# Kernel optimization log

Measured on AMD Instinct MI355X. Metric: run time of the kernel, lower is better.

## Reference

```python
import jax, jax.numpy as jnp
import numpy as np

B, N, P, K = 128, 256, 256, 4  # batches, obs points, pred points, nfunc


def setup_inputs() -> dict:
    key = jax.random.key(0)
    k1, k2, k3, k4, k5 = jax.random.split(key, 5)
    # squared distances: symmetric obs-obs block with zero diagonal + obs-pred block
    d_oo = jax.random.uniform(k1, (B, N, N), dtype=jnp.float32) * 25.0
    d_oo = 0.5 * (d_oo + jnp.swapaxes(d_oo, -1, -2))
    d_oo = d_oo * (1.0 - jnp.eye(N, dtype=jnp.float32))
    d_op = jax.random.uniform(k2, (B, N, P), dtype=jnp.float32) * 25.0
    C = jnp.concatenate([d_oo, d_op], axis=-1)  # (B, N, N+P)
    val = jax.random.normal(k3, (B, N, K), dtype=jnp.float32)
    bad = jax.random.randint(k4, (B, N), 0, 10) == 0
    rm = jax.random.normal(k5, (K, 1), dtype=jnp.float32) * 0.1  # MyKF.rm param
    eps_param = -1.5 * jnp.ones((K,), dtype=jnp.float32)          # DistOA.eps param
    return {"C": C, "val": val, "rm": rm, "eps_param": eps_param, "bad": bad}


def _forward(C, val, rm, eps_param, bad):
    n = C.shape[-2]
    # MyKF: x = d2 * sigmoid(rm)/rmax^2 (rmax=1); kernel (1+x)exp(-x)  -> (K,B,n,n+p)
    rmk = jax.nn.sigmoid(rm)[..., None, None]            # (K,1,1,1)
    x = rmk * C[None]
    Cf = (1.0 + x) * jnp.exp(-x)                          # (K,B,n,n+p)
    b = Cf[..., n:]                                       # (K,B,n,p)
    Cm = Cf[..., :n]                                      # (K,B,n,n)
    # implicit: add sigmoid(eps) on the diagonal
    eps = jax.nn.sigmoid(eps_param)[:, None, None, None]  # (K,1,1,1)
    Cm = Cm + eps * jnp.eye(n, dtype=C.dtype)
    # NaN/bad masking: zero bad rows of b; zero xor(bad_i, bad_j) entries of C
    good = (~bad).astype(C.dtype)                         # (B,n)
    b = b * good[None, :, :, None]
    keep = (~(bad[:, :, None] ^ bad[:, None, :])).astype(C.dtype)  # (B,n,n)
    Cm = Cm * keep[None]
    # batched solve + clamp-based reweighting (edging=False)
    d = jnp.linalg.solve(Cm, b)                           # (K,B,n,p)
    wg = jnp.clip((jnp.abs(d).sum(-2, keepdims=True) - 1.0) * 2.0, 0.0, 1.0)
    d1 = b / Cm.sum(-1, keepdims=True)
    r = d * (1.0 - wg) + d1 * (wg / jnp.clip(d1.sum(-2, keepdims=True), 1.0, None))
    # neddvalgrad=False -> val detached before nan_to_num
    val0 = jnp.nan_to_num(jax.lax.stop_gradient(val))     # (B,n,K)
    return jnp.einsum('kbjp,bjk->bpk', r, val0)           # (B,p,K)


def reference(C, val, rm, eps_param, bad):
    return _forward(C, val, rm, eps_param, bad)
```

## Files before the change

### kernel.cpp

```cpp
#include <hip/hip_runtime.h>
#include <cstddef>

#define NN 256
#define PP 256
#define BB 128
#define KK 4
#define NSYS 512
#define PW 32
#define NPAN (NN/PW)

__device__ __forceinline__ float sigmoidf_(float x){ return 1.0f/(1.0f+expf(-x)); }

__global__ __launch_bounds__(256) void build_kernel(
    const float* __restrict__ C, const float* __restrict__ rm,
    const float* __restrict__ epsp, const int* __restrict__ bad,
    float* __restrict__ A, float* __restrict__ rowsum, int s0)
{
  const int si = blockIdx.x;
  const int ls = si >> 8;
  const int i  = si & 255;
  const int s  = s0 + ls;
  const int k  = s >> 7;
  const int b  = s & 127;
  const int j  = threadIdx.x;

  const float sk = sigmoidf_(rm[k]);
  const float ek = sigmoidf_(epsp[k]);
  const bool bad_i = bad[b*NN + i] != 0;
  const bool bad_j = bad[b*NN + j] != 0;

  float c  = C[((size_t)b*NN + i)*(NN+PP) + j];
  float x  = sk * c;
  float cf = (1.0f + x) * expf(-x);
  if (i == j) cf += ek;
  float keep = (bad_i == bad_j) ? 1.0f : 0.0f;
  float a = cf * keep;
  A[((size_t)ls*NN + i)*NN + j] = a;

  __shared__ float red[256];
  red[j] = a; __syncthreads();
  #pragma unroll
  for (int off = 128; off > 0; off >>= 1){
    if (j < off) red[j] += red[j + off];
    __syncthreads();
  }
  if (j == 0) rowsum[ls*NN + i] = red[0];
}

__global__ __launch_bounds__(512, 4) void lu_kernel(
    float* __restrict__ Aall, int* __restrict__ permAll)
{
  __shared__ float panel[NN][PW+1];
  __shared__ float linv[PW][PW+1];
  __shared__ float uinv[PW][PW+1];
  __shared__ float urow[PW][NN-PW];
  __shared__ float redv[2][8];
  __shared__ int   redi[2][8];
  __shared__ int   pivseq[NN];
  __shared__ int   actlist[NN];
  __shared__ unsigned char pickedsh[NN];
  __shared__ int   nact;

  const int ls = blockIdx.x;
  float* __restrict__ A = Aall + (size_t)ls*NN*NN;
  const int t = threadIdx.x;
  const int lane = t & 63, wid = t >> 6;
  bool picked = false;
  if (t < NN) pickedsh[t] = 0;

  for (int I = 0; I < NPAN; ++I){
    const int col0 = I*PW;
    const int W = NN - col0 - PW;
    if (t == 0) nact = 0;
    __syncthreads();

    for (int e = t; e < NN*PW; e += 512){
      int r = e >> 5, c = e & 31;
      panel[r][c] = A[(size_t)r*NN + col0 + c];
    }
    __syncthreads();

    {
      float v = -1.0f; int vi = 0;
      if (t < NN && !picked){ v = fabsf(panel[t][0]); vi = t; }
      #pragma unroll
      for (int off = 32; off > 0; off >>= 1){
        float ov = __shfl_down(v, off); int oi = __shfl_down(vi, off);
        if (ov > v){ v = ov; vi = oi; }
      }
      if (lane == 0){ redv[0][wid] = v; redi[0][wid] = vi; }
    }
    __syncthreads();

    for (int c = 0; c < PW; ++c){
      const int par = c & 1;
      float bv = redv[par][0]; int p = redi[par][0];
      #pragma unroll
      for (int w = 1; w < 8; ++w)
        if (redv[par][w] > bv){ bv = redv[par][w]; p = redi[par][w]; }
      if (t == p){ picked = true; pickedsh[t] = 1; pivseq[col0+c] = t; }

      float nv = -1.0f; int ni = t;
      if (t < NN && !picked){
        const float rdia = 1.0f / panel[p][c];
        float m = panel[t][c] * rdia;
        panel[t][c] = m;
        float nxt = -1.0f;
        #pragma unroll
        for (int j = 0; j < PW; ++j){
          if (j > c){
            float u = panel[t][j] - m * panel[p][j];
            panel[t][j] = u;
            if (j == c+1) nxt = fabsf(u);
          }
        }
        nv = nxt;
      }
      #pragma unroll
      for (int off = 32; off > 0; off >>= 1){
        float ov = __shfl_down(nv, off); int oi = __shfl_down(ni, off);
        if (ov > nv){ nv = ov; ni = oi; }
      }
      if (lane == 0){ redv[par^1][wid] = nv; redi[par^1][wid] = ni; }
      __syncthreads();
    }

    if (t >= 256){
      const int jj = t - 256;
      if (jj < W){
        const int j = col0 + PW + jj;
        float u[PW];
        #pragma unroll
        for (int c = 0; c < PW; ++c) u[c] = A[(size_t)pivseq[col0+c]*NN + j];
        #pragma unroll
        for (int c = 0; c < PW; ++c){
          const int pc = pivseq[col0+c];
          float sv = u[c];
          #pragma unroll
          for (int k2 = 0; k2 < PW; ++k2)
            if (k2 < c) sv -= panel[pc][k2] * u[k2];
          u[c] = sv;
          urow[c][jj] = sv;
          A[(size_t)pc*NN + j] = sv;
        }
      }
    } else if (t < PW){
      const int cth = t;
      for (int r = cth; r < PW; ++r){
        float sv = (r == cth) ? 1.0f : 0.0f;
        const int pr = pivseq[col0+r];
        for (int k2 = cth; k2 < r; ++k2) sv -= panel[pr][k2] * linv[k2][cth];
        linv[r][cth] = sv;
      }
    } else if (t >= 64 && t < 64+PW){
      const int cth = t - 64;
      for (int r = cth; r >= 0; --r){
        float sv = (r == cth) ? 1.0f : 0.0f;
        const int pr = pivseq[col0+r];
        for (int k2 = r+1; k2 <= cth; ++k2) sv -= panel[pr][k2] * uinv[k2][cth];
        uinv[r][cth] = sv / panel[pr][r];
      }
    } else if (t >= 128 && t < 192){
      #pragma unroll
      for (int q = 0; q < 4; ++q){
        int r = (t-128)*4 + q;
        if (!pickedsh[r]){ int pos = atomicAdd(&nact, 1); actlist[pos] = r; }
      }
    }
    __syncthreads();

    for (int e = t; e < PW*PW; e += 512){
      int r = e >> 5, c2 = e & 31;
      A[(size_t)pivseq[col0+r]*NN + col0 + c2] = (r > c2) ? linv[r][c2] : uinv[r][c2];
    }
    for (int e = t; e < NN*PW; e += 512){
      int r = e >> 5, c2 = e & 31;
      if (!pickedsh[r]) A[(size_t)r*NN + col0 + c2] = panel[r][c2];
    }

    if (W > 0){
      for (int i0 = wid*2; i0 < W; i0 += 16){
        const int r0 = actlist[i0];
        const int r1 = actlist[i0+1];
        float4* R0 = (float4*)(A + (size_t)r0*NN + col0 + PW);
        float4* R1 = (float4*)(A + (size_t)r1*NN + col0 + PW);
        if (lane*4 < W){
          float4 a0 = R0[lane];
          float4 a1 = R1[lane];
          #pragma unroll
          for (int c = 0; c < PW; ++c){
            float4 u4 = *(const float4*)&urow[c][lane*4];
            float p0 = panel[r0][c], p1 = panel[r1][c];
            a0.x -= p0*u4.x; a0.y -= p0*u4.y; a0.z -= p0*u4.z; a0.w -= p0*u4.w;
            a1.x -= p1*u4.x; a1.y -= p1*u4.y; a1.z -= p1*u4.z; a1.w -= p1*u4.w;
          }
          R0[lane] = a0;
          R1[lane] = a1;
        }
      }
    }
  }
  __syncthreads();
  if (t < NN) permAll[ls*NN + t] = pivseq[t];
}

__global__ __launch_bounds__(512) void solve_epi_kernel(
    const float* __restrict__ Aall, const int* __restrict__ permAll,
    const float* __restrict__ rowsum,
    const float* __restrict__ C, const float* __restrict__ val,
    const int* __restrict__ bad, const float* __restrict__ rm,
    float* __restrict__ out, int s0)
{
  __shared__ float tile[NN][128];
  __shared__ float dblk[PW][PW+1];
  __shared__ __align__(16) float ubuf[4096];
  __shared__ int   perm[NN];

  int ls, c0;
  {
    const int g = blockIdx.x;
    if ((gridDim.x & 15) == 0){
      const int xcd = g & 7, idx = g >> 3;
      ls = xcd + 8*(idx >> 1);
      c0 = (idx & 1) * 128;
    } else {
      ls = g >> 1;
      c0 = (g & 1) * 128;
    }
  }
  const int s  = s0 + ls;
  const int k  = s >> 7, b = s & 127;
  const float* __restrict__ A = Aall + (size_t)ls*NN*NN;
  const float* __restrict__ rs = rowsum + ls*NN;
  const int t = threadIdx.x;
  const int lane = t & 63, wid = t >> 6;
  const int lane2 = lane + 64;
  const float sk = sigmoidf_(rm[k]);
  const int slr = t >> 3;
  const int sq4 = (t & 7) << 2;

  if (t < NN) perm[t] = permAll[ls*NN + t];
  __syncthreads();

  for (int e = t; e < NN*128; e += 512){
    int i = e >> 7, c = e & 127;
    int pi = perm[i];
    float cb = C[((size_t)b*NN + pi)*(NN+PP) + NN + c0 + c];
    float xb = sk * cb;
    float bf = (1.0f + xb) * expf(-xb);
    if (bad[b*NN + pi]) bf = 0.0f;
    tile[i][c] = bf;
  }
  __syncthreads();

  for (int J = 0; J < NPAN; ++J){
    const int j0 = J*PW;
    for (int e = t; e < PW*PW; e += 512){
      int r = e >> 5, c = e & 31;
      dblk[r][c] = A[(size_t)perm[j0+r]*NN + j0 + c];
    }
    __syncthreads();
    const int r0 = wid*4;
    float ya0 = tile[j0+r0+0][lane],  yb0 = tile[j0+r0+0][lane2];
    float ya1 = tile[j0+r0+1][lane],  yb1 = tile[j0+r0+1][lane2];
    float ya2 = tile[j0+r0+2][lane],  yb2 = tile[j0+r0+2][lane2];
    float ya3 = tile[j0+r0+3][lane],  yb3 = tile[j0+r0+3][lane2];
    for (int kk = 0; kk < r0; ++kk){
      float xa = tile[j0+kk][lane], xb = tile[j0+kk][lane2];
      float d0 = dblk[r0+0][kk], d1 = dblk[r0+1][kk], d2 = dblk[r0+2][kk], d3 = dblk[r0+3][kk];
      ya0 += d0*xa; yb0 += d0*xb;
      ya1 += d1*xa; yb1 += d1*xb;
      ya2 += d2*xa; yb2 += d2*xb;
      ya3 += d3*xa; yb3 += d3*xb;
    }
    {
      float xa0 = tile[j0+r0][lane],  xa1 = tile[j0+r0+1][lane],  xa2 = tile[j0+r0+2][lane];
      float xb0 = tile[j0+r0][lane2], xb1 = tile[j0+r0+1][lane2], xb2 = tile[j0+r0+2][lane2];
      float e10 = dblk[r0+1][r0];
      float e20 = dblk[r0+2][r0], e21 = dblk[r0+2][r0+1];
      float e30 = dblk[r0+3][r0], e31 = dblk[r0+3][r0+1], e32 = dblk[r0+3][r0+2];
      ya1 += e10*xa0;                         yb1 += e10*xb0;
      ya2 += e20*xa0 + e21*xa1;               yb2 += e20*xb0 + e21*xb1;
      ya3 += e30*xa0 + e31*xa1 + e32*xa2;     yb3 += e30*xb0 + e31*xb1 + e32*xb2;
    }
    __syncthreads();
    tile[j0+r0+0][lane]=ya0; tile[j0+r0+0][lane2]=yb0;
    tile[j0+r0+1][lane]=ya1; tile[j0+r0+1][lane2]=yb1;
    tile[j0+r0+2][lane]=ya2; tile[j0+r0+2][lane2]=yb2;
    tile[j0+r0+3][lane]=ya3; tile[j0+r0+3][lane2]=yb3;
    __syncthreads();
    const int nbelow = NN - j0 - PW;
    if (nbelow > 0){
      float xa[PW], xb[PW];
      #pragma unroll
      for (int kk = 0; kk < PW; ++kk){ xa[kk] = tile[j0+kk][lane]; xb[kk] = tile[j0+kk][lane2]; }
      for (int cb2 = 0; cb2 < nbelow; cb2 += 64){
        const int rows_c = (nbelow - cb2 < 64) ? (nbelow - cb2) : 64;
        if (t < rows_c*8)
          *(float4*)&ubuf[(slr<<5) + sq4] =
            *(const float4*)(A + (size_t)perm[j0+PW+cb2+slr]*NN + j0 + sq4);
        __syncthreads();
        const int rpw = rows_c >> 3;
        for (int p2 = 0; p2 < rpw; p2 += 2){
          const int lr0 = wid*rpw + p2;
          const int ia = j0 + PW + cb2 + lr0, ib = ia + 1;
          const float* __restrict__ S0 = &ubuf[lr0<<5];
          const float* __restrict__ S1 = &ubuf[(lr0+1)<<5];
          float a0a = tile[ia][lane], a0b = tile[ia][lane2];
          float a1a = tile[ib][lane], a1b = tile[ib][lane2];
          #pragma unroll
          for (int q = 0; q < 8; ++q){
            float4 a4 = *(const float4*)(S0 + (q<<2));
            float4 b4 = *(const float4*)(S1 + (q<<2));
            a0a -= a4.x*xa[q*4+0] + a4.y*xa[q*4+1] + a4.z*xa[q*4+2] + a4.w*xa[q*4+3];
            a0b -= a4.x*xb[q*4+0] + a4.y*xb[q*4+1] + a4.z*xb[q*4+2] + a4.w*xb[q*4+3];
            a1a -= b4.x*xa[q*4+0] + b4.y*xa[q*4+1] + b4.z*xa[q*4+2] + b4.w*xa[q*4+3];
            a1b -= b4.x*xb[q*4+0] + b4.y*xb[q*4+1] + b4.z*xb[q*4+2] + b4.w*xb[q*4+3];
          }
          tile[ia][lane] = a0a; tile[ia][lane2] = a0b;
          tile[ib][lane] = a1a; tile[ib][lane2] = a1b;
        }
        __syncthreads();
      }
    }
  }

  for (int J = NPAN-1; J >= 0; --J){
    const int j0 = J*PW;
    for (int e = t; e < PW*PW; e += 512){
      int r = e >> 5, c = e & 31;
      dblk[r][c] = A[(size_t)perm[j0+r]*NN + j0 + c];
    }
    __syncthreads();
    const int r0 = wid*4;
    float ya0=0.f, ya1=0.f, ya2=0.f, ya3=0.f;
    float yb0=0.f, yb1=0.f, yb2=0.f, yb3=0.f;
    for (int kk = r0+4; kk < PW; ++kk){
      float xa = tile[j0+kk][lane], xb = tile[j0+kk][lane2];
      float d0 = dblk[r0+0][kk], d1 = dblk[r0+1][kk], d2 = dblk[r0+2][kk], d3 = dblk[r0+3][kk];
      ya0 += d0*xa; yb0 += d0*xb;
      ya1 += d1*xa; yb1 += d1*xb;
      ya2 += d2*xa; yb2 += d2*xb;
      ya3 += d3*xa; yb3 += d3*xb;
    }
    {
      float xa0 = tile[j0+r0][lane],  xa1 = tile[j0+r0+1][lane];
      float xa2 = tile[j0+r0+2][lane], xa3 = tile[j0+r0+3][lane];
      float xb0 = tile[j0+r0][lane2],  xb1 = tile[j0+r0+1][lane2];
      float xb2 = tile[j0+r0+2][lane2], xb3 = tile[j0+r0+3][lane2];
      float e00=dblk[r0][r0], e01=dblk[r0][r0+1], e02=dblk[r0][r0+2], e03=dblk[r0][r0+3];
      float e11=dblk[r0+1][r0+1], e12=dblk[r0+1][r0+2], e13=dblk[r0+1][r0+3];
      float e22=dblk[r0+2][r0+2], e23=dblk[r0+2][r0+3];
      float e33=dblk[r0+3][r0+3];
      ya0 += e00*xa0 + e01*xa1 + e02*xa2 + e03*xa3;  yb0 += e00*xb0 + e01*xb1 + e02*xb2 + e03*xb3;
      ya1 += e11*xa1 + e12*xa2 + e13*xa3;            yb1 += e11*xb1 + e12*xb2 + e13*xb3;
      ya2 += e22*xa2 + e23*xa3;                      yb2 += e22*xb2 + e23*xb3;
      ya3 += e33*xa3;                                yb3 += e33*xb3;
    }
    __syncthreads();
    tile[j0+r0+0][lane]=ya0; tile[j0+r0+0][lane2]=yb0;
    tile[j0+r0+1][lane]=ya1; tile[j0+r0+1][lane2]=yb1;
    tile[j0+r0+2][lane]=ya2; tile[j0+r0+2][lane2]=yb2;
    tile[j0+r0+3][lane]=ya3; tile[j0+r0+3][lane2]=yb3;
    __syncthreads();
    if (j0 > 0){
      float xa[PW], xb[PW];
      #pragma unroll
      for (int kk = 0; kk < PW; ++kk){ xa[kk] = tile[j0+kk][lane]; xb[kk] = tile[j0+kk][lane2]; }
      for (int cb2 = 0; cb2 < j0; cb2 += 64){
        const int rows_c = (j0 - cb2 < 64) ? (j0 - cb2) : 64;
        if (t < rows_c*8)
          *(float4*)&ubuf[(slr<<5) + sq4] =
            *(const float4*)(A + (size_t)perm[cb2+slr]*NN + j0 + sq4);
        __syncthreads();
        const int rpw = rows_c >> 3;
        for (int p2 = 0; p2 < rpw; p2 += 2){
          const int lr0 = wid*rpw + p2;
          const int ia = cb2 + lr0, ib = ia + 1;
          const float* __restrict__ S0 = &ubuf[lr0<<5];
          const float* __restrict__ S1 = &ubuf[(lr0+1)<<5];
          float a0a = tile[ia][lane], a0b = tile[ia][lane2];
          float a1a = tile[ib][lane], a1b = tile[ib][lane2];
          #pragma unroll
          for (int q = 0; q < 8; ++q){
            float4 a4 = *(const float4*)(S0 + (q<<2));
            float4 b4 = *(const float4*)(S1 + (q<<2));
            a0a -= a4.x*xa[q*4+0] + a4.y*xa[q*4+1] + a4.z*xa[q*4+2] + a4.w*xa[q*4+3];
            a0b -= a4.x*xb[q*4+0] + a4.y*xb[q*4+1] + a4.z*xb[q*4+2] + a4.w*xb[q*4+3];
            a1a -= b4.x*xa[q*4+0] + b4.y*xa[q*4+1] + b4.z*xa[q*4+2] + b4.w*xa[q*4+3];
            a1b -= b4.x*xb[q*4+0] + b4.y*xb[q*4+1] + b4.z*xb[q*4+2] + b4.w*xb[q*4+3];
          }
          tile[ia][lane] = a0a; tile[ia][lane2] = a0b;
          tile[ib][lane] = a1a; tile[ib][lane2] = a1b;
        }
        __syncthreads();
      }
    }
  }

  {
    float sdva=0.f, sabsa=0.f, s1va=0.f, s1a=0.f;
    float sdvb=0.f, sabsb=0.f, s1vb=0.f, s1b=0.f;
    const int pa = c0 + lane, pb = c0 + lane2;
    for (int j = wid*32; j < wid*32 + 32; ++j){
      float v = val[(b*NN + j)*KK + k];
      if (v != v) v = 0.0f;
      const float rsj = rs[j];
      const bool bj = bad[b*NN + j] != 0;
      float da = tile[j][lane];
      float cba = C[((size_t)b*NN + j)*(NN+PP) + NN + pa];
      float xba = sk*cba;
      float boa = (1.0f+xba)*expf(-xba);
      if (bj) boa = 0.0f;
      float d1a = boa / rsj;
      sdva += da*v; sabsa += fabsf(da); s1va += d1a*v; s1a += d1a;
      float db = tile[j][lane2];
      float cbb = C[((size_t)b*NN + j)*(NN+PP) + NN + pb];
      float xbb = sk*cbb;
      float bob = (1.0f+xbb)*expf(-xbb);
      if (bj) bob = 0.0f;
      float d1b = bob / rsj;
      sdvb += db*v; sabsb += fabsf(db); s1vb += d1b*v; s1b += d1b;
    }
    __syncthreads();
    ubuf[(0*8 + wid)*128 + lane] = sdva;  ubuf[(0*8 + wid)*128 + lane2] = sdvb;
    ubuf[(1*8 + wid)*128 + lane] = sabsa; ubuf[(1*8 + wid)*128 + lane2] = sabsb;
    ubuf[(2*8 + wid)*128 + lane] = s1va;  ubuf[(2*8 + wid)*128 + lane2] = s1vb;
    ubuf[(3*8 + wid)*128 + lane] = s1a;   ubuf[(3*8 + wid)*128 + lane2] = s1b;
  }
  __syncthreads();
  if (t < 128){
    float sdv=0.f, sabs=0.f, s1v=0.f, s1=0.f;
    #pragma unroll
    for (int w = 0; w < 8; ++w){
      sdv  += ubuf[(0*8 + w)*128 + t];
      sabs += ubuf[(1*8 + w)*128 + t];
      s1v  += ubuf[(2*8 + w)*128 + t];
      s1   += ubuf[(3*8 + w)*128 + t];
    }
    float wg    = fminf(fmaxf((sabs - 1.0f)*2.0f, 0.0f), 1.0f);
    float denom = fmaxf(s1, 1.0f);
    out[((size_t)b*PP + c0 + t)*KK + k] = (1.0f - wg)*sdv + (wg/denom)*s1v;
  }
}

extern "C" void kernel_launch(void* const* d_in, const int* in_sizes, int n_in,
                              void* d_out, int out_size, void* d_ws, size_t ws_size,
                              hipStream_t stream)
{
  (void)in_sizes; (void)n_in; (void)out_size;
  const float* C    = (const float*)d_in[0];
  const float* val  = (const float*)d_in[1];
  const float* rm   = (const float*)d_in[2];
  const float* epsp = (const float*)d_in[3];
  const int*   bad  = (const int*)d_in[4];
  float* out = (float*)d_out;

  const size_t per_sys = (size_t)NN*NN*4 + (size_t)NN*4 + (size_t)NN*4;
  int chunk = (int)(ws_size / per_sys);
  if (chunk < 1)    chunk = 1;
  if (chunk > NSYS) chunk = NSYS;

  float* ws     = (float*)d_ws;
  float* A      = ws;
  float* rowsum = A + (size_t)chunk*NN*NN;
  int*   perm   = (int*)(rowsum + (size_t)chunk*NN);

  for (int s0 = 0; s0 < NSYS; s0 += chunk){
    int cs = (NSYS - s0 < chunk) ? (NSYS - s0) : chunk;
    build_kernel<<<cs*NN, 256, 0, stream>>>(C, rm, epsp, bad, A, rowsum, s0);
    lu_kernel<<<cs, 512, 0, stream>>>(A, perm);
    solve_epi_kernel<<<cs*2, 512, 0, stream>>>(A, perm, rowsum, C, val, bad, rm, out, s0);
  }
}
```

Measured before the change: 1.530 ms.

## Keep LU panel rows in registers during pivot factorization

During panel factorization each thread now holds its 32-element panel row in registers, loaded with float4 global reads, instead of reading and writing the shared panel every column. The pivot row is broadcast through a small shared buffer, and the panel is written back to shared memory once after the column loop for the triangular solves. This removes repeated shared-memory traffic in the serial per-column loop but adds an extra barrier per column. The min-blocks hint in launch_bounds is dropped, so the compiler may use more registers and lower occupancy.

```diff
diff --git a/kernel.cpp b/kernel.cpp
--- a/kernel.cpp
+++ b/kernel.cpp
@@ -8,6 +8,7 @@
 #define NSYS 512
 #define PW 32
 #define NPAN (NN/PW)
+#define PSTR 36
 
 __device__ __forceinline__ float sigmoidf_(float x){ return 1.0f/(1.0f+expf(-x)); }
 
@@ -47,10 +48,11 @@
   if (j == 0) rowsum[ls*NN + i] = red[0];
 }
 
-__global__ __launch_bounds__(512, 4) void lu_kernel(
+__global__ __launch_bounds__(512) void lu_kernel(
     float* __restrict__ Aall, int* __restrict__ permAll)
 {
-  __shared__ float panel[NN][PW+1];
+  __shared__ __align__(16) float panel[NN][PSTR];
+  __shared__ __align__(16) float prow[PSTR];
   __shared__ float linv[PW][PW+1];
   __shared__ float uinv[PW][PW+1];
   __shared__ float urow[PW][NN-PW];
@@ -74,15 +76,19 @@
     if (t == 0) nact = 0;
     __syncthreads();
 
-    for (int e = t; e < NN*PW; e += 512){
-      int r = e >> 5, c = e & 31;
-      panel[r][c] = A[(size_t)r*NN + col0 + c];
-    }
-    __syncthreads();
+    float u[PW];
+    if (t < NN){
+      const float4* Ar = (const float4*)(A + (size_t)t*NN + col0);
+      float4 q0=Ar[0],q1=Ar[1],q2=Ar[2],q3=Ar[3],q4=Ar[4],q5=Ar[5],q6=Ar[6],q7=Ar[7];
+      u[0]=q0.x;u[1]=q0.y;u[2]=q0.z;u[3]=q0.w;   u[4]=q1.x;u[5]=q1.y;u[6]=q1.z;u[7]=q1.w;
+      u[8]=q2.x;u[9]=q2.y;u[10]=q2.z;u[11]=q2.w; u[12]=q3.x;u[13]=q3.y;u[14]=q3.z;u[15]=q3.w;
+      u[16]=q4.x;u[17]=q4.y;u[18]=q4.z;u[19]=q4.w;u[20]=q5.x;u[21]=q5.y;u[22]=q5.z;u[23]=q5.w;
+      u[24]=q6.x;u[25]=q6.y;u[26]=q6.z;u[27]=q6.w;u[28]=q7.x;u[29]=q7.y;u[30]=q7.z;u[31]=q7.w;
+    }
 
     {
-      float v = -1.0f; int vi = 0;
-      if (t < NN && !picked){ v = fabsf(panel[t][0]); vi = t; }
+      float v = -1.0f; int vi = t;
+      if (t < NN && !picked) v = fabsf(u[0]);
       #pragma unroll
       for (int off = 32; off > 0; off >>= 1){
         float ov = __shfl_down(v, off); int oi = __shfl_down(vi, off);
@@ -98,23 +104,45 @@
       #pragma unroll
       for (int w = 1; w < 8; ++w)
         if (redv[par][w] > bv){ bv = redv[par][w]; p = redi[par][w]; }
-      if (t == p){ picked = true; pickedsh[t] = 1; pivseq[col0+c] = t; }
+      if (t == p){
+        picked = true; pickedsh[t] = 1; pivseq[col0+c] = t;
+        float4* Pw = (float4*)prow;
+        Pw[0]=make_float4(u[0],u[1],u[2],u[3]);     Pw[1]=make_float4(u[4],u[5],u[6],u[7]);
+        Pw[2]=make_float4(u[8],u[9],u[10],u[11]);   Pw[3]=make_float4(u[12],u[13],u[14],u[15]);
+        Pw[4]=make_float4(u[16],u[17],u[18],u[19]); Pw[5]=make_float4(u[20],u[21],u[22],u[23]);
+        Pw[6]=make_float4(u[24],u[25],u[26],u[27]); Pw[7]=make_float4(u[28],u[29],u[30],u[31]);
+        float pd = u[0];
+        #pragma unroll
+        for (int j = 1; j < PW; ++j) if (j == c) pd = u[j];
+        prow[32] = pd;
+      }
+      __syncthreads();
 
       float nv = -1.0f; int ni = t;
-      if (t < NN && !picked){
-        const float rdia = 1.0f / panel[p][c];
-        float m = panel[t][c] * rdia;
-        panel[t][c] = m;
-        float nxt = -1.0f;
-        #pragma unroll
-        for (int j = 0; j < PW; ++j){
-          if (j > c){
-            float u = panel[t][j] - m * panel[p][j];
-            panel[t][j] = u;
-            if (j == c+1) nxt = fabsf(u);
+      if (t < NN){
+        float pr[PW];
+        {
+          const float4* Pr = (const float4*)prow;
+          float4 p0=Pr[0],p1=Pr[1],p2=Pr[2],p3=Pr[3],p4=Pr[4],p5=Pr[5],p6=Pr[6],p7=Pr[7];
+          pr[0]=p0.x;pr[1]=p0.y;pr[2]=p0.z;pr[3]=p0.w;   pr[4]=p1.x;pr[5]=p1.y;pr[6]=p1.z;pr[7]=p1.w;
+          pr[8]=p2.x;pr[9]=p2.y;pr[10]=p2.z;pr[11]=p2.w; pr[12]=p3.x;pr[13]=p3.y;pr[14]=p3.z;pr[15]=p3.w;
+          pr[16]=p4.x;pr[17]=p4.y;pr[18]=p4.z;pr[19]=p4.w;pr[20]=p5.x;pr[21]=p5.y;pr[22]=p5.z;pr[23]=p5.w;
+          pr[24]=p6.x;pr[25]=p6.y;pr[26]=p6.z;pr[27]=p6.w;pr[28]=p7.x;pr[29]=p7.y;pr[30]=p7.z;pr[31]=p7.w;
+        }
+        const float rdia = 1.0f / prow[32];
+        if (!picked){
+          float uc = u[0];
+          #pragma unroll
+          for (int j = 1; j < PW; ++j) if (j == c) uc = u[j];
+          const float m = uc * rdia;
+          #pragma unroll
+          for (int j = 0; j < PW; ++j){
+            if (j > c)       u[j] = u[j] - m * pr[j];
+            else if (j == c) u[j] = m;
           }
+          #pragma unroll
+          for (int j = 0; j < PW; ++j) if (j == c+1) nv = fabsf(u[j]);
         }
-        nv = nxt;
       }
       #pragma unroll
       for (int off = 32; off > 0; off >>= 1){
@@ -125,21 +153,30 @@
       __syncthreads();
     }
 
+    if (t < NN){
+      float4* Pp = (float4*)&panel[t][0];
+      Pp[0]=make_float4(u[0],u[1],u[2],u[3]);     Pp[1]=make_float4(u[4],u[5],u[6],u[7]);
+      Pp[2]=make_float4(u[8],u[9],u[10],u[11]);   Pp[3]=make_float4(u[12],u[13],u[14],u[15]);
+      Pp[4]=make_float4(u[16],u[17],u[18],u[19]); Pp[5]=make_float4(u[20],u[21],u[22],u[23]);
+      Pp[6]=make_float4(u[24],u[25],u[26],u[27]); Pp[7]=make_float4(u[28],u[29],u[30],u[31]);
+    }
+    __syncthreads();
+
     if (t >= 256){
       const int jj = t - 256;
       if (jj < W){
         const int j = col0 + PW + jj;
-        float u[PW];
+        float uu[PW];
         #pragma unroll
-        for (int c = 0; c < PW; ++c) u[c] = A[(size_t)pivseq[col0+c]*NN + j];
+        for (int c = 0; c < PW; ++c) uu[c] = A[(size_t)pivseq[col0+c]*NN + j];
         #pragma unroll
         for (int c = 0; c < PW; ++c){
           const int pc = pivseq[col0+c];
-          float sv = u[c];
+          float sv = uu[c];
           #pragma unroll
           for (int k2 = 0; k2 < PW; ++k2)
-            if (k2 < c) sv -= panel[pc][k2] * u[k2];
-          u[c] = sv;
+            if (k2 < c) sv -= panel[pc][k2] * uu[k2];
+          uu[c] = sv;
           urow[c][jj] = sv;
           A[(size_t)pc*NN + j] = sv;
         }
@@ -148,17 +185,17 @@
       const int cth = t;
       for (int r = cth; r < PW; ++r){
         float sv = (r == cth) ? 1.0f : 0.0f;
-        const int pr = pivseq[col0+r];
-        for (int k2 = cth; k2 < r; ++k2) sv -= panel[pr][k2] * linv[k2][cth];
+        const int pr2 = pivseq[col0+r];
+        for (int k2 = cth; k2 < r; ++k2) sv -= panel[pr2][k2] * linv[k2][cth];
         linv[r][cth] = sv;
       }
     } else if (t >= 64 && t < 64+PW){
       const int cth = t - 64;
       for (int r = cth; r >= 0; --r){
         float sv = (r == cth) ? 1.0f : 0.0f;
-        const int pr = pivseq[col0+r];
-        for (int k2 = r+1; k2 <= cth; ++k2) sv -= panel[pr][k2] * uinv[k2][cth];
-        uinv[r][cth] = sv / panel[pr][r];
+        const int pr2 = pivseq[col0+r];
+        for (int k2 = r+1; k2 <= cth; ++k2) sv -= panel[pr2][k2] * uinv[k2][cth];
+        uinv[r][cth] = sv / panel[pr2][r];
       }
     } else if (t >= 128 && t < 192){
       #pragma unroll
```

Result: slower. 3.000 ms (+96.1%).
